# Kernel tuning notes

Measured on AMD Instinct MI355X. Metric: run time of the kernel, lower is better.

The kernel has to match this reference:

```python
import jax, jax.numpy as jnp
import numpy as np

B, N, C = 128, 2048, 256
H, OUT = 8, 256
KD = C // H   # per-head key dim = 32
VD = C // H   # per-head value dim = 32


def _glorot(key, shape):
    fan_in, fan_out = shape[0], int(np.prod(shape[1:]))
    limit = np.sqrt(3.0 * 2.0 / (fan_in + fan_out))
    return jax.random.uniform(key, shape, jnp.float32, -limit, limit)


def setup_inputs() -> dict:
    key = jax.random.key(0)
    ks = jax.random.split(key, 8)
    q_data = jax.random.normal(ks[0], (B, N, C), jnp.float32)
    m_data = jax.random.normal(ks[1], (B, N, C), jnp.float32)
    q_mask = jnp.ones((B, N, 1), jnp.float32)
    bias = jnp.zeros((B, 1, N), jnp.float32)  # ignored by module (overwritten)
    query_w = _glorot(ks[2], (C, H, KD))
    key_w = _glorot(ks[3], (C, KD))            # keys share a single head projection
    value_w = _glorot(ks[4], (C, VD))
    gating_w = jnp.zeros((C, H, VD), jnp.float32)   # Constant(0) init as in source
    gating_b = jnp.ones((H, VD), jnp.float32)       # Constant(1) init as in source
    output_w = _glorot(ks[5], (H, VD, OUT))         # zero_init=False -> glorot
    output_b = jnp.zeros((OUT,), jnp.float32)
    return dict(q_data=q_data, m_data=m_data, q_mask=q_mask, bias=bias,
                query_w=query_w, key_w=key_w, value_w=value_w,
                gating_w=gating_w, gating_b=gating_b,
                output_w=output_w, output_b=output_b)


def reference(q_data, m_data, q_mask, bias, query_w, key_w, value_w,
              gating_w, gating_b, output_w, output_b):
    key_dim = query_w.shape[-1]
    # value/key projections (single shared head dim for k, v)
    v = jnp.einsum('bka,ac->bkc', m_data, value_w)          # [B,N,VD]
    k = jnp.einsum('bka,ac->bkc', m_data, key_w)            # [B,N,KD]
    # masked mean pooling over queries -> single pooled query per batch
    q_avg = jnp.sum(q_mask * q_data, axis=1) / (jnp.sum(q_mask, axis=1) + 1e-10)  # [B,C]
    q = jnp.einsum('ba,ahc->bhc', q_avg, query_w) * key_dim ** (-0.5)             # [B,H,KD]
    attn_bias = 1e9 * (q_mask[:, None, :, 0] - 1.0)         # [B,1,N]
    logits = jnp.einsum('bhc,bkc->bhk', q, k) + attn_bias   # [B,H,N]
    weights = jax.nn.softmax(logits, axis=-1)
    weighted_avg = jnp.einsum('bhk,bkc->bhc', weights, v)   # [B,H,VD]
    # sigmoid gating per query position
    gate = jax.nn.sigmoid(jnp.einsum('bqc,chv->bqhv', q_data, gating_w) + gating_b)  # [B,N,H,VD]
    gated = weighted_avg[:, None] * gate                    # [B,N,H,VD]
    output = jnp.einsum('bqhc,hco->bqo', gated, output_w) + output_b  # [B,N,OUT]
    return output
```

## Files before the change

kernel.cpp:

```cpp
#include <hip/hip_runtime.h>
#include <hip/hip_bf16.h>
#include <math.h>


typedef unsigned short u16;
typedef u16 us4 __attribute__((ext_vector_type(4)));
typedef short bf16x8 __attribute__((ext_vector_type(8)));
typedef float f32x4 __attribute__((ext_vector_type(4)));

static __device__ __forceinline__ u16 f2bf(float f) {
    union { float f; unsigned int u; } x; x.f = f;
    unsigned int u = x.u;
    return (u16)((u + 0x7FFFu + ((u >> 16) & 1u)) >> 16);
}
static __device__ __forceinline__ float bf2f(u16 h) {
    union { unsigned int u; float f; } x; x.u = ((unsigned int)h) << 16;
    return x.f;
}

static __device__ __forceinline__ bf16x8 ldfrag(const u16* p) {
    us4 lo = *(const us4*)p;
    us4 hi = *(const us4*)(p + 16);
    bf16x8 a;
    a[0] = (short)lo[0]; a[1] = (short)lo[1]; a[2] = (short)lo[2]; a[3] = (short)lo[3];
    a[4] = (short)hi[0]; a[5] = (short)hi[1]; a[6] = (short)hi[2]; a[7] = (short)hi[3];
    return a;
}

__global__ void k0_prep(const float* __restrict__ gating_w,
                        const float* __restrict__ output_w,
                        const float* __restrict__ key_w,
                        const float* __restrict__ value_w,
                        u16* __restrict__ WT1, u16* __restrict__ WT2,
                        u16* __restrict__ WKVT) {
    int i = blockIdx.x * 256 + threadIdx.x;
    if (i < 65536) {
        int a = i >> 8, j = i & 255;
        WT1[j * 256 + a] = f2bf(gating_w[i]);
    } else if (i < 131072) {
        int i2 = i - 65536; int j = i2 >> 8, o = i2 & 255;
        WT2[o * 256 + j] = f2bf(output_w[i2]);
    } else if (i < 139264) {
        int i2 = i - 131072; int a = i2 >> 5, n = i2 & 31;
        WKVT[n * 256 + a] = f2bf(key_w[i2]);
    } else if (i < 147456) {
        int i2 = i - 139264; int a = i2 >> 5, n = i2 & 31;
        WKVT[(32 + n) * 256 + a] = f2bf(value_w[i2]);
    }
}

__global__ __launch_bounds__(256) void k1a_qsum(const float* __restrict__ qd,
                                                const float* __restrict__ qmask,
                                                float* __restrict__ qsum,
                                                float* __restrict__ msum) {
    int b = blockIdx.x >> 3, ch = blockIdx.x & 7;
    int t = threadIdx.x;
    __shared__ float ml[256];
    int n0 = b * 2048 + ch * 256;
    ml[t] = qmask[n0 + t];
    __syncthreads();
    float acc = 0.f;
    for (int r = 0; r < 256; ++r)
        acc += ml[r] * qd[(long)(n0 + r) * 256 + t];
    atomicAdd(&qsum[b * 256 + t], acc);
    __syncthreads();
    for (int s = 128; s > 0; s >>= 1) {
        if (t < s) ml[t] += ml[t + s];
        __syncthreads();
    }
    if (t == 0) atomicAdd(&msum[b], ml[0]);
}

__global__ __launch_bounds__(256) void k1b_qproj(const float* __restrict__ qsum,
                                                 const float* __restrict__ msum,
                                                 const float* __restrict__ query_w,
                                                 float* __restrict__ qproj) {
    int b = blockIdx.x, t = threadIdx.x;
    __shared__ float sq[256];
    float denom = msum[b] + 1e-10f;
    sq[t] = qsum[b * 256 + t] / denom;
    __syncthreads();
    float acc = 0.f;
    for (int c = 0; c < 256; ++c)
        acc += sq[c] * query_w[c * 256 + t];
    qproj[b * 256 + t] = acc * 0.17677669529663687f;
}

#define MS_STR 260
__global__ __launch_bounds__(256) void k2_kv(const float* __restrict__ md,
                                             const u16* __restrict__ WKVT,
                                             u16* __restrict__ kk,
                                             u16* __restrict__ vv) {
    __shared__ u16 ms[64 * MS_STR];
    int t = threadIdx.x;
    long base = (long)blockIdx.x * 64;
    const float4* md4 = (const float4*)md + base * 64;
    for (int i = t; i < 4096; i += 256) {
        int r = i >> 6, c4 = i & 63;
        float4 v = md4[r * 64 + c4];
        us4 u; u[0] = f2bf(v.x); u[1] = f2bf(v.y); u[2] = f2bf(v.z); u[3] = f2bf(v.w);
        *(us4*)&ms[r * MS_STR + c4 * 4] = u;
    }
    __syncthreads();
    int w = t >> 6, l = t & 63, lg = l >> 4, ln = l & 15;
    int m0 = w * 16;
    f32x4 acc[4] = {};
#pragma unroll
    for (int ks = 0; ks < 8; ++ks) {
        int k0 = ks * 32;
        bf16x8 a = ldfrag(&ms[(m0 + ln) * MS_STR + k0 + 4 * lg]);
#pragma unroll
        for (int nt = 0; nt < 4; ++nt) {
            bf16x8 bb = ldfrag(&WKVT[(nt * 16 + ln) * 256 + k0 + 4 * lg]);
            acc[nt] = __builtin_amdgcn_mfma_f32_16x16x32_bf16(a, bb, acc[nt], 0, 0, 0);
        }
    }
#pragma unroll
    for (int nt = 0; nt < 4; ++nt) {
        int n = nt * 16 + ln;
#pragma unroll
        for (int rr = 0; rr < 4; ++rr) {
            long row = base + m0 + lg * 4 + rr;
            u16 vb = f2bf(acc[nt][rr]);
            if (n < 32) kk[row * 32 + n] = vb;
            else        vv[row * 32 + (n - 32)] = vb;
        }
    }
}

__global__ __launch_bounds__(256) void k3_attn(const float* __restrict__ qproj,
                                               const u16* __restrict__ kk,
                                               const u16* __restrict__ vv,
                                               const float* __restrict__ qmask,
                                               float* __restrict__ wa) {
    int b = blockIdx.x >> 3, h = blockIdx.x & 7;
    int t = threadIdx.x;
    __shared__ float qh[32];
    __shared__ float red[256];
    __shared__ float vred[256 * 33];
    if (t < 32) qh[t] = qproj[b * 256 + h * 32 + t];
    __syncthreads();
    float er[8];
    float lmax = -1e30f;
#pragma unroll
    for (int i = 0; i < 8; ++i) {
        int n = t + i * 256;
        const us4* kr = (const us4*)(kk + (size_t)(b * 2048 + n) * 32);
        float acc = 1e9f * (qmask[b * 2048 + n] - 1.0f);
#pragma unroll
        for (int j = 0; j < 8; ++j) {
            us4 u = kr[j];
            acc += qh[j * 4 + 0] * bf2f(u[0]) + qh[j * 4 + 1] * bf2f(u[1])
                 + qh[j * 4 + 2] * bf2f(u[2]) + qh[j * 4 + 3] * bf2f(u[3]);
        }
        er[i] = acc;
        lmax = fmaxf(lmax, acc);
    }
    red[t] = lmax; __syncthreads();
    for (int s = 128; s > 0; s >>= 1) {
        if (t < s) red[t] = fmaxf(red[t], red[t + s]);
        __syncthreads();
    }
    float M = red[0];
    __syncthreads();
    float esum = 0.f;
#pragma unroll
    for (int i = 0; i < 8; ++i) { er[i] = expf(er[i] - M); esum += er[i]; }
    red[t] = esum; __syncthreads();
    for (int s = 128; s > 0; s >>= 1) {
        if (t < s) red[t] += red[t + s];
        __syncthreads();
    }
    float S = red[0];
    __syncthreads();
    float vacc[32];
#pragma unroll
    for (int j = 0; j < 32; ++j) vacc[j] = 0.f;
#pragma unroll
    for (int i = 0; i < 8; ++i) {
        int n = t + i * 256;
        const us4* vr = (const us4*)(vv + (size_t)(b * 2048 + n) * 32);
        float wgt = er[i];
#pragma unroll
        for (int j = 0; j < 8; ++j) {
            us4 u = vr[j];
            vacc[j * 4 + 0] += wgt * bf2f(u[0]);
            vacc[j * 4 + 1] += wgt * bf2f(u[1]);
            vacc[j * 4 + 2] += wgt * bf2f(u[2]);
            vacc[j * 4 + 3] += wgt * bf2f(u[3]);
        }
    }
#pragma unroll
    for (int j = 0; j < 32; ++j) vred[t * 33 + j] = vacc[j];
    __syncthreads();
    for (int s = 128; s > 0; s >>= 1) {
        if (t < s) {
#pragma unroll
            for (int j = 0; j < 32; ++j) vred[t * 33 + j] += vred[(t + s) * 33 + j];
        }
        __syncthreads();
    }
    if (t < 32) wa[b * 256 + h * 32 + t] = vred[t] / S;
}

#define QSTR 260
__global__ __launch_bounds__(256) void k4_out(const float* __restrict__ qd,
                                              const u16* __restrict__ WT1,
                                              const u16* __restrict__ WT2,
                                              const float* __restrict__ wa,
                                              const float* __restrict__ gating_b,
                                              const float* __restrict__ output_b,
                                              float* __restrict__ out) {
    __shared__ u16 qs[64 * QSTR];
    int t = threadIdx.x;
    long base = (long)blockIdx.x * 64;
    int b = blockIdx.x >> 5;
    const float4* q4 = (const float4*)qd + base * 64;
    for (int i = t; i < 4096; i += 256) {
        int r = i >> 6, c4 = i & 63;
        float4 v = q4[r * 64 + c4];
        us4 u; u[0] = f2bf(v.x); u[1] = f2bf(v.y); u[2] = f2bf(v.z); u[3] = f2bf(v.w);
        *(us4*)&qs[r * QSTR + c4 * 4] = u;
    }
    __syncthreads();
    int w = t >> 6, l = t & 63, lg = l >> 4, ln = l & 15;

    f32x4 acc[4][4] = {};
#pragma unroll
    for (int ks = 0; ks < 8; ++ks) {
        int k0 = ks * 32;
        bf16x8 a[4];
#pragma unroll
        for (int mt = 0; mt < 4; ++mt)
            a[mt] = ldfrag(&qs[(mt * 16 + ln) * QSTR + k0 + 4 * lg]);
#pragma unroll
        for (int nt = 0; nt < 4; ++nt) {
            int col = w * 64 + nt * 16 + ln;
            bf16x8 bb = ldfrag(&WT1[col * 256 + k0 + 4 * lg]);
#pragma unroll
            for (int mt = 0; mt < 4; ++mt)
                acc[mt][nt] = __builtin_amdgcn_mfma_f32_16x16x32_bf16(a[mt], bb, acc[mt][nt], 0, 0, 0);
        }
    }
    __syncthreads();

#pragma unroll
    for (int nt = 0; nt < 4; ++nt) {
        int col = w * 64 + nt * 16 + ln;
        float gb = gating_b[col];
        float wv = wa[b * 256 + col];
#pragma unroll
        for (int mt = 0; mt < 4; ++mt) {
#pragma unroll
            for (int rr = 0; rr < 4; ++rr) {
                float x = acc[mt][nt][rr];
                float gt = 1.0f / (1.0f + expf(-(x + gb)));
                int row = mt * 16 + lg * 4 + rr;
                qs[row * QSTR + col] = f2bf(wv * gt);
            }
        }
    }
    __syncthreads();

    f32x4 acc2[4][4] = {};
#pragma unroll
    for (int ks = 0; ks < 8; ++ks) {
        int k0 = ks * 32;
        bf16x8 a[4];
#pragma unroll
        for (int mt = 0; mt < 4; ++mt)
            a[mt] = ldfrag(&qs[(mt * 16 + ln) * QSTR + k0 + 4 * lg]);
#pragma unroll
        for (int nt = 0; nt < 4; ++nt) {
            int o = w * 64 + nt * 16 + ln;
            bf16x8 bb = ldfrag(&WT2[o * 256 + k0 + 4 * lg]);
#pragma unroll
            for (int mt = 0; mt < 4; ++mt)
                acc2[mt][nt] = __builtin_amdgcn_mfma_f32_16x16x32_bf16(a[mt], bb, acc2[mt][nt], 0, 0, 0);
        }
    }
#pragma unroll
    for (int nt = 0; nt < 4; ++nt) {
        int o = w * 64 + nt * 16 + ln;
        float ob = output_b[o];
#pragma unroll
        for (int mt = 0; mt < 4; ++mt) {
#pragma unroll
            for (int rr = 0; rr < 4; ++rr) {
                long row = base + mt * 16 + lg * 4 + rr;
                out[row * 256 + o] = acc2[mt][nt][rr] + ob;
            }
        }
    }
}

extern "C" void kernel_launch(void* const* d_in, const int* in_sizes, int n_in,
                              void* d_out, int out_size, void* d_ws, size_t ws_size,
                              hipStream_t stream) {
    const float* q_data   = (const float*)d_in[0];
    const float* m_data   = (const float*)d_in[1];
    const float* q_mask   = (const float*)d_in[2];
    const float* query_w  = (const float*)d_in[4];
    const float* key_w    = (const float*)d_in[5];
    const float* value_w  = (const float*)d_in[6];
    const float* gating_w = (const float*)d_in[7];
    const float* gating_b = (const float*)d_in[8];
    const float* output_w = (const float*)d_in[9];
    const float* output_b = (const float*)d_in[10];
    float* out = (float*)d_out;

    char* ws = (char*)d_ws;
    u16*   WT1   = (u16*)(ws);
    u16*   WT2   = (u16*)(ws + 131072);
    u16*   WKVT  = (u16*)(ws + 262144);
    float* qsum  = (float*)(ws + 294912);
    float* msum  = (float*)(ws + 425984);
    float* qproj = (float*)(ws + 426496);
    float* wa    = (float*)(ws + 557568);
    u16*   kk    = (u16*)(ws + 688640);
    u16*   vv    = (u16*)(ws + 688640 + 16777216);

    hipMemsetAsync(ws + 294912, 0, 131584, stream);
    k0_prep<<<576, 256, 0, stream>>>(gating_w, output_w, key_w, value_w, WT1, WT2, WKVT);
    k1a_qsum<<<1024, 256, 0, stream>>>(q_data, q_mask, qsum, msum);
    k1b_qproj<<<128, 256, 0, stream>>>(qsum, msum, query_w, qproj);
    k2_kv<<<4096, 256, 0, stream>>>(m_data, WKVT, kk, vv);
    k3_attn<<<1024, 256, 0, stream>>>(qproj, kk, vv, q_mask, wa);
    k4_out<<<4096, 256, 0, stream>>>(q_data, WT1, WT2, wa, gating_b, output_b, out);
}
```

Baseline: 1.057 ms.

## Pre-swizzle weights and q_data into MFMA fragment layout, fuse bf16 staging into qsum

Weights are pre-packed in k0_prep into the exact per-lane MFMA fragment order, so the GEMM kernels load B operands as single 16-byte vector loads instead of two strided 8-byte loads. When the workspace is large enough, the qsum kernel also writes a bf16 copy of q_data in fragment order, and k4_out reads A fragments straight from global memory without staging fp32 q_data through LDS. This trades an extra 128MB bf16 write plus reread for removing the fp32 reread and conversion in k4. Sigmoid and softmax now use __expf and a hardware reciprocal instead of the precise versions.

```diff
diff --git a/kernel.cpp b/kernel.cpp
--- a/kernel.cpp
+++ b/kernel.cpp
@@ -19,34 +19,95 @@
 }
 
 static __device__ __forceinline__ bf16x8 ldfrag(const u16* p) {
-    us4 lo = *(const us4*)p;
-    us4 hi = *(const us4*)(p + 16);
-    bf16x8 a;
-    a[0] = (short)lo[0]; a[1] = (short)lo[1]; a[2] = (short)lo[2]; a[3] = (short)lo[3];
-    a[4] = (short)hi[0]; a[5] = (short)hi[1]; a[6] = (short)hi[2]; a[7] = (short)hi[3];
-    return a;
+    union { bf16x8 v; struct { us4 lo, hi; } s; } u;
+    u.s.lo = *(const us4*)p;
+    u.s.hi = *(const us4*)(p + 16);
+    return u.v;
 }
 
 __global__ void k0_prep(const float* __restrict__ gating_w,
                         const float* __restrict__ output_w,
                         const float* __restrict__ key_w,
                         const float* __restrict__ value_w,
-                        u16* __restrict__ WT1, u16* __restrict__ WT2,
-                        u16* __restrict__ WKVT) {
+                        u16* __restrict__ W1F, u16* __restrict__ W2F,
+                        u16* __restrict__ WKVTF) {
     int i = blockIdx.x * 256 + threadIdx.x;
-    if (i < 65536) {
-        int a = i >> 8, j = i & 255;
-        WT1[j * 256 + a] = f2bf(gating_w[i]);
-    } else if (i < 131072) {
-        int i2 = i - 65536; int j = i2 >> 8, o = i2 & 255;
-        WT2[o * 256 + j] = f2bf(output_w[i2]);
-    } else if (i < 139264) {
-        int i2 = i - 131072; int a = i2 >> 5, n = i2 & 31;
-        WKVT[n * 256 + a] = f2bf(key_w[i2]);
+    if (i < 131072) {
+        int e = i & 65535;
+        int frag = e >> 9, l = (e >> 3) & 63, j = e & 7;
+        int ln = l & 15, lg = l >> 4, half = j >> 2, jj = j & 3;
+        int col = ((frag >> 3) << 4) + ln;
+        int k   = ((frag & 7) << 5) + (half << 4) + (lg << 2) + jj;
+        const float* src = (i < 65536) ? gating_w : output_w;
+        u16* dst = (i < 65536) ? W1F : W2F;
+        dst[e] = f2bf(src[k * 256 + col]);
     } else if (i < 147456) {
-        int i2 = i - 139264; int a = i2 >> 5, n = i2 & 31;
-        WKVT[(32 + n) * 256 + a] = f2bf(value_w[i2]);
-    }
+        int e = i - 131072;
+        int frag = e >> 9, l = (e >> 3) & 63, j = e & 7;
+        int ln = l & 15, lg = l >> 4, half = j >> 2, jj = j & 3;
+        int n = ((frag >> 3) << 4) + ln;
+        int k = ((frag & 7) << 5) + (half << 4) + (lg << 2) + jj;
+        WKVTF[e] = f2bf(n < 32 ? key_w[k * 32 + n] : value_w[k * 32 + (n - 32)]);
+    }
+}
+
+#define TS_STR 260
+__global__ __launch_bounds__(256) void k1a_fuse(const float* __restrict__ qd,
+                                                const float* __restrict__ qmask,
+                                                u16* __restrict__ qbfF,
+                                                float* __restrict__ qsum,
+                                                float* __restrict__ msum) {
+    __shared__ float ml[256];
+    __shared__ u16 ts[64 * TS_STR];
+    __shared__ float csum[4][256];
+    int t = threadIdx.x;
+    int b = blockIdx.x >> 3, chunk = blockIdx.x & 7;
+    int n0 = b * 2048 + chunk * 256;
+    ml[t] = qmask[n0 + t];
+    int rl = t >> 6, c4 = t & 63;
+    float a0 = 0.f, a1 = 0.f, a2 = 0.f, a3 = 0.f;
+    const float4* qd4 = (const float4*)qd;
+    us4* qbf4 = (us4*)qbfF;
+    __syncthreads();
+    for (int sub = 0; sub < 4; ++sub) {
+        us4 myv[16];
+#pragma unroll
+        for (int j = 0; j < 16; ++j) {
+            int row = j * 4 + rl;
+            float4 v = qd4[(size_t)(n0 + sub * 64 + row) * 64 + c4];
+            float m = ml[sub * 64 + row];
+            a0 += m * v.x; a1 += m * v.y; a2 += m * v.z; a3 += m * v.w;
+            us4 u; u[0] = f2bf(v.x); u[1] = f2bf(v.y); u[2] = f2bf(v.z); u[3] = f2bf(v.w);
+            myv[j] = u;
+        }
+        __syncthreads();
+#pragma unroll
+        for (int j = 0; j < 16; ++j) {
+            int row = j * 4 + rl;
+            *(us4*)&ts[row * TS_STR + c4 * 4] = myv[j];
+        }
+        __syncthreads();
+        int tile = blockIdx.x * 4 + sub;
+#pragma unroll
+        for (int j = 0; j < 16; ++j) {
+            int u = j * 256 + t;
+            int frag = u >> 7, l = (u >> 1) & 63, half = u & 1;
+            int ln = l & 15, lg = l >> 4, mt = frag >> 3, ks = frag & 7;
+            int srow = mt * 16 + ln;
+            int scol = ks * 32 + half * 16 + lg * 4;
+            qbf4[(size_t)tile * 4096 + u] = *(const us4*)&ts[srow * TS_STR + scol];
+        }
+    }
+    csum[rl][c4 * 4 + 0] = a0; csum[rl][c4 * 4 + 1] = a1;
+    csum[rl][c4 * 4 + 2] = a2; csum[rl][c4 * 4 + 3] = a3;
+    __syncthreads();
+    float s = csum[0][t] + csum[1][t] + csum[2][t] + csum[3][t];
+    atomicAdd(&qsum[b * 256 + t], s);
+    for (int st = 128; st > 0; st >>= 1) {
+        if (t < st) ml[t] += ml[t + st];
+        __syncthreads();
+    }
+    if (t == 0) atomicAdd(&msum[b], ml[0]);
 }
 
 __global__ __launch_bounds__(256) void k1a_qsum(const float* __restrict__ qd,
@@ -88,7 +149,7 @@
 
 #define MS_STR 260
 __global__ __launch_bounds__(256) void k2_kv(const float* __restrict__ md,
-                                             const u16* __restrict__ WKVT,
+                                             const u16* __restrict__ WKVTF,
                                              u16* __restrict__ kk,
                                              u16* __restrict__ vv) {
     __shared__ u16 ms[64 * MS_STR];
@@ -104,6 +165,7 @@
     __syncthreads();
     int w = t >> 6, l = t & 63, lg = l >> 4, ln = l & 15;
     int m0 = w * 16;
+    const bf16x8* wkv = (const bf16x8*)WKVTF;
     f32x4 acc[4] = {};
 #pragma unroll
     for (int ks = 0; ks < 8; ++ks) {
@@ -111,7 +173,7 @@
         bf16x8 a = ldfrag(&ms[(m0 + ln) * MS_STR + k0 + 4 * lg]);
 #pragma unroll
         for (int nt = 0; nt < 4; ++nt) {
-            bf16x8 bb = ldfrag(&WKVT[(nt * 16 + ln) * 256 + k0 + 4 * lg]);
+            bf16x8 bb = wkv[(nt * 8 + ks) * 64 + l];
             acc[nt] = __builtin_amdgcn_mfma_f32_16x16x32_bf16(a, bb, acc[nt], 0, 0, 0);
         }
     }
@@ -165,7 +227,7 @@
     __syncthreads();
     float esum = 0.f;
 #pragma unroll
-    for (int i = 0; i < 8; ++i) { er[i] = expf(er[i] - M); esum += er[i]; }
+    for (int i = 0; i < 8; ++i) { er[i] = __expf(er[i] - M); esum += er[i]; }
     red[t] = esum; __syncthreads();
     for (int s = 128; s > 0; s >>= 1) {
         if (t < s) red[t] += red[t + s];
@@ -203,40 +265,121 @@
     if (t < 32) wa[b * 256 + h * 32 + t] = vred[t] / S;
 }
 
-#define QSTR 260
-__global__ __launch_bounds__(256) void k4_out(const float* __restrict__ qd,
-                                              const u16* __restrict__ WT1,
-                                              const u16* __restrict__ WT2,
+#define PSTR 264
+__global__ __launch_bounds__(256) void k4_out(const u16* __restrict__ qbfF,
+                                              const u16* __restrict__ W1F,
+                                              const u16* __restrict__ W2F,
                                               const float* __restrict__ wa,
                                               const float* __restrict__ gating_b,
                                               const float* __restrict__ output_b,
                                               float* __restrict__ out) {
-    __shared__ u16 qs[64 * QSTR];
-    int t = threadIdx.x;
-    long base = (long)blockIdx.x * 64;
-    int b = blockIdx.x >> 5;
+    __shared__ u16 ps[64 * PSTR];
+    int t = threadIdx.x;
+    int tile = blockIdx.x;
+    int b = tile >> 5;
+    int w = t >> 6, l = t & 63, lg = l >> 4, ln = l & 15;
+    const bf16x8* qa = (const bf16x8*)(qbfF + (size_t)tile * 16384);
+    const bf16x8* w1 = (const bf16x8*)W1F;
+    const bf16x8* w2 = (const bf16x8*)W2F;
+
+    f32x4 acc[4][4] = {};
+#pragma unroll
+    for (int ks = 0; ks < 8; ++ks) {
+        bf16x8 a[4];
+#pragma unroll
+        for (int mt = 0; mt < 4; ++mt)
+            a[mt] = qa[(mt * 8 + ks) * 64 + l];
+#pragma unroll
+        for (int nt = 0; nt < 4; ++nt) {
+            bf16x8 bb = w1[((w * 4 + nt) * 8 + ks) * 64 + l];
+#pragma unroll
+            for (int mt = 0; mt < 4; ++mt)
+                acc[mt][nt] = __builtin_amdgcn_mfma_f32_16x16x32_bf16(a[mt], bb, acc[mt][nt], 0, 0, 0);
+        }
+    }
+
+#pragma unroll
+    for (int nt = 0; nt < 4; ++nt) {
+        int col = w * 64 + nt * 16 + ln;
+        float gb = gating_b[col];
+        float wv = wa[b * 256 + col];
+#pragma unroll
+        for (int mt = 0; mt < 4; ++mt) {
+#pragma unroll
+            for (int rr = 0; rr < 4; ++rr) {
+                float x = acc[mt][nt][rr] + gb;
+                float e = __expf(-x);
+                float p = wv * __builtin_amdgcn_rcpf(1.0f + e);
+                ps[(mt * 16 + lg * 4 + rr) * PSTR + col] = f2bf(p);
+            }
+        }
+    }
+    __syncthreads();
+
+    f32x4 acc2[4][4] = {};
+#pragma unroll
+    for (int ks = 0; ks < 8; ++ks) {
+        bf16x8 a[4];
+#pragma unroll
+        for (int mt = 0; mt < 4; ++mt)
+            a[mt] = ldfrag(&ps[(mt * 16 + ln) * PSTR + ks * 32 + 4 * lg]);
+#pragma unroll
+        for (int nt = 0; nt < 4; ++nt) {
+            bf16x8 bb = w2[((w * 4 + nt) * 8 + ks) * 64 + l];
+#pragma unroll
+            for (int mt = 0; mt < 4; ++mt)
+                acc2[mt][nt] = __builtin_amdgcn_mfma_f32_16x16x32_bf16(a[mt], bb, acc2[mt][nt], 0, 0, 0);
+        }
+    }
+#pragma unroll
+    for (int nt = 0; nt < 4; ++nt) {
+        int o = w * 64 + nt * 16 + ln;
+        float ob = output_b[o];
+#pragma unroll
+        for (int mt = 0; mt < 4; ++mt) {
+#pragma unroll
+            for (int rr = 0; rr < 4; ++rr) {
+                size_t row = (size_t)tile * 64 + mt * 16 + lg * 4 + rr;
+                out[row * 256 + o] = acc2[mt][nt][rr] + ob;
+            }
+        }
+    }
+}
+
+__global__ __launch_bounds__(256) void k4_stage(const float* __restrict__ qd,
+                                                const u16* __restrict__ W1F,
+                                                const u16* __restrict__ W2F,
+                                                const float* __restrict__ wa,
+                                                const float* __restrict__ gating_b,
+                                                const float* __restrict__ output_b,
+                                                float* __restrict__ out) {
+    __shared__ u16 qs[64 * PSTR];
+    int t = threadIdx.x;
+    int tile = blockIdx.x;
+    long base = (long)tile * 64;
+    int b = tile >> 5;
     const float4* q4 = (const float4*)qd + base * 64;
     for (int i = t; i < 4096; i += 256) {
         int r = i >> 6, c4 = i & 63;
         float4 v = q4[r * 64 + c4];
         us4 u; u[0] = f2bf(v.x); u[1] = f2bf(v.y); u[2] = f2bf(v.z); u[3] = f2bf(v.w);
-        *(us4*)&qs[r * QSTR + c4 * 4] = u;
+        *(us4*)&qs[r * PSTR + c4 * 4] = u;
     }
     __syncthreads();
     int w = t >> 6, l = t & 63, lg = l >> 4, ln = l & 15;
+    const bf16x8* w1 = (const bf16x8*)W1F;
+    const bf16x8* w2 = (const bf16x8*)W2F;
 
     f32x4 acc[4][4] = {};
 #pragma unroll
     for (int ks = 0; ks < 8; ++ks) {
-        int k0 = ks * 32;
         bf16x8 a[4];
 #pragma unroll
         for (int mt = 0; mt < 4; ++mt)
-            a[mt] = ldfrag(&qs[(mt * 16 + ln) * QSTR + k0 + 4 * lg]);
+            a[mt] = ldfrag(&qs[(mt * 16 + ln) * PSTR + ks * 32 + 4 * lg]);
 #pragma unroll
         for (int nt = 0; nt < 4; ++nt) {
-            int col = w * 64 + nt * 16 + ln;
-            bf16x8 bb = ldfrag(&WT1[col * 256 + k0 + 4 * lg]);
+            bf16x8 bb = w1[((w * 4 + nt) * 8 + ks) * 64 + l];
 #pragma unroll
             for (int mt = 0; mt < 4; ++mt)
                 acc[mt][nt] = __builtin_amdgcn_mfma_f32_16x16x32_bf16(a[mt], bb, acc[mt][nt], 0, 0, 0);
@@ -253,10 +396,10 @@
         for (int mt = 0; mt < 4; ++mt) {
 #pragma unroll
             for (int rr = 0; rr < 4; ++rr) {
-                float x = acc[mt][nt][rr];
-                float gt = 1.0f / (1.0f + expf(-(x + gb)));
-                int row = mt * 16 + lg * 4 + rr;
-                qs[row * QSTR + col] = f2bf(wv * gt);
+                float x = acc[mt][nt][rr] + gb;
+                float e = __expf(-x);
+                float p = wv * __builtin_amdgcn_rcpf(1.0f + e);
+                qs[(mt * 16 + lg * 4 + rr) * PSTR + col] = f2bf(p);
             }
         }
     }
@@ -265,15 +408,13 @@
     f32x4 acc2[4][4] = {};
 #pragma unroll
     for (int ks = 0; ks < 8; ++ks) {
-        int k0 = ks * 32;
         bf16x8 a[4];
 #pragma unroll
         for (int mt = 0; mt < 4; ++mt)
-            a[mt] = ldfrag(&qs[(mt * 16 + ln) * QSTR + k0 + 4 * lg]);
+            a[mt] = ldfrag(&qs[(mt * 16 + ln) * PSTR + ks * 32 + 4 * lg]);
 #pragma unroll
         for (int nt = 0; nt < 4; ++nt) {
-            int o = w * 64 + nt * 16 + ln;
-            bf16x8 bb = ldfrag(&WT2[o * 256 + k0 + 4 * lg]);
+            bf16x8 bb = w2[((w * 4 + nt) * 8 + ks) * 64 + l];
 #pragma unroll
             for (int mt = 0; mt < 4; ++mt)
                 acc2[mt][nt] = __builtin_amdgcn_mfma_f32_16x16x32_bf16(a[mt], bb, acc2[mt][nt], 0, 0, 0);
@@ -287,7 +428,7 @@
         for (int mt = 0; mt < 4; ++mt) {
 #pragma unroll
             for (int rr = 0; rr < 4; ++rr) {
-                long row = base + mt * 16 + lg * 4 + rr;
+                size_t row = base + mt * 16 + lg * 4 + rr;
                 out[row * 256 + o] = acc2[mt][nt][rr] + ob;
             }
         }
@@ -310,21 +451,33 @@
     float* out = (float*)d_out;
 
     char* ws = (char*)d_ws;
-    u16*   WT1   = (u16*)(ws);
-    u16*   WT2   = (u16*)(ws + 131072);
-    u16*   WKVT  = (u16*)(ws + 262144);
+    u16*   W1F   = (u16*)(ws);
+    u16*   W2F   = (u16*)(ws + 131072);
+    u16*   WKVTF = (u16*)(ws + 262144);
     float* qsum  = (float*)(ws + 294912);
     float* msum  = (float*)(ws + 425984);
     float* qproj = (float*)(ws + 426496);
     float* wa    = (float*)(ws + 557568);
     u16*   kk    = (u16*)(ws + 688640);
     u16*   vv    = (u16*)(ws + 688640 + 16777216);
+    u16*   qbfF  = (u16*)(ws + 688640 + 2 * 16777216);
+
+    const size_t NEED_BIG = 688640 + 2ull * 16777216 + 134217728;
+    bool big = ws_size >= NEED_BIG;
 
     hipMemsetAsync(ws + 294912, 0, 131584, stream);
-    k0_prep<<<576, 256, 0, stream>>>(gating_w, output_w, key_w, value_w, WT1, WT2, WKVT);
-    k1a_qsum<<<1024, 256, 0, stream>>>(q_data, q_mask, qsum, msum);
+    k0_prep<<<576, 256, 0, stream>>>(gating_w, output_w, key_w, value_w, W1F, W2F, WKVTF);
+    if (big) {
+        k1a_fuse<<<1024, 256, 0, stream>>>(q_data, q_mask, qbfF, qsum, msum);
+    } else {
+        k1a_qsum<<<1024, 256, 0, stream>>>(q_data, q_mask, qsum, msum);
+    }
     k1b_qproj<<<128, 256, 0, stream>>>(qsum, msum, query_w, qproj);
-    k2_kv<<<4096, 256, 0, stream>>>(m_data, WKVT, kk, vv);
+    k2_kv<<<4096, 256, 0, stream>>>(m_data, WKVTF, kk, vv);
     k3_attn<<<1024, 256, 0, stream>>>(qproj, kk, vv, q_mask, wa);
-    k4_out<<<4096, 256, 0, stream>>>(q_data, WT1, WT2, wa, gating_b, output_b, out);
-}
+    if (big) {
+        k4_out<<<4096, 256, 0, stream>>>(qbfF, W1F, W2F, wa, gating_b, output_b, out);
+    } else {
+        k4_stage<<<4096, 256, 0, stream>>>(q_data, W1F, W2F, wa, gating_b, output_b, out);
+    }
+}
```

After: 864.5 us. 1.22x faster.
